# Kernel tuning notes

Hardware: AMD Instinct MI355X
Metric: run time of the kernel (lower is better)

Reference implementation:

```python
import jax, jax.numpy as jnp
import numpy as np

N_QUBITS = 4
N_LAYERS = 6
BATCH = 131072

# Pauli-Z expectation sign table: qubit q corresponds to bit (N_QUBITS-1-q) of the
# flattened state index (axis q+1 of the [B,2,2,2,2] state is most-significant first).
_idx = np.arange(2 ** N_QUBITS)
Z_SIGNS = jnp.asarray(1.0 - 2.0 * ((_idx[:, None] >> (N_QUBITS - 1 - np.arange(N_QUBITS))) & 1), dtype=jnp.float32)  # [16, 4]


def _apply_1q(state, U, q):
    # state: [B, 2,2,2,2]; U: [2,2] (shared) or [B,2,2] (per-sample)
    s = jnp.moveaxis(state, q + 1, -1)
    if U.ndim == 3:
        s = jnp.einsum('bij,b...j->b...i', U, s)
    else:
        s = jnp.einsum('ij,b...j->b...i', U, s)
    return jnp.moveaxis(s, -1, q + 1)


def _apply_cnot(state, c, t):
    # flip target axis on the control=1 slice
    s = jnp.moveaxis(state, (c + 1, t + 1), (-2, -1))
    s = jnp.concatenate([s[..., :1, :], s[..., 1:, ::-1]], axis=-2)
    return jnp.moveaxis(s, (-2, -1), (c + 1, t + 1))


def _rot(phi, theta, omega):
    # PennyLane Rot(phi, theta, omega) = RZ(omega) @ RY(theta) @ RZ(phi)
    ct = jnp.cos(theta / 2)
    st = jnp.sin(theta / 2)
    ep = jnp.exp(-0.5j * (phi + omega))  # e^{-i(phi+omega)/2}
    em = jnp.exp(0.5j * (phi - omega))   # e^{ i(phi-omega)/2}
    row0 = jnp.stack([ep * ct, -em * st])
    row1 = jnp.stack([jnp.conj(em) * st, jnp.conj(ep) * ct])
    return jnp.stack([row0, row1]).astype(jnp.complex64)


def _forward(inputs, rotations):
    B = inputs.shape[0]
    # |0...0> batched state
    state = jnp.zeros((B,) + (2,) * N_QUBITS, dtype=jnp.complex64)
    state = state.at[(slice(None),) + (0,) * N_QUBITS].set(1.0)

    # AngleEmbedding: RX(x_q) on wire q (per-sample gates)
    c = jnp.cos(inputs / 2)
    s = jnp.sin(inputs / 2)
    for q in range(N_QUBITS):
        U = jnp.stack([
            jnp.stack([c[:, q] + 0j, -1j * s[:, q]], axis=-1),
            jnp.stack([-1j * s[:, q], c[:, q] + 0j], axis=-1),
        ], axis=-2).astype(jnp.complex64)  # [B,2,2]
        state = _apply_1q(state, U, q)

    # StronglyEntanglingLayers
    for l in range(N_LAYERS):
        for q in range(N_QUBITS):
            state = _apply_1q(state, _rot(rotations[l, q, 0], rotations[l, q, 1], rotations[l, q, 2]), q)
        r = l % (N_QUBITS - 1) + 1  # default imprimitive range pattern
        for q in range(N_QUBITS):
            state = _apply_cnot(state, q, (q + r) % N_QUBITS)

    probs = (state.real ** 2 + state.imag ** 2).reshape(B, 2 ** N_QUBITS)  # [B,16]
    return (probs @ Z_SIGNS).astype(jnp.float32)  # [B, N_QUBITS] = <Z_q>


def setup_inputs() -> dict:
    key = jax.random.key(0)
    k1, k2 = jax.random.split(key)
    inputs = jax.random.normal(k1, (BATCH, N_QUBITS), dtype=jnp.float32)
    # keras 'random_uniform' initializer: U(-0.05, 0.05)
    rotations = jax.random.uniform(k2, (N_LAYERS, N_QUBITS, 3), dtype=jnp.float32, minval=-0.05, maxval=0.05)
    return {"inputs": inputs, "rotations": rotations}


def reference(inputs, rotations):
    return _forward(inputs, rotations)
```

## Files before the change

### kernel.cpp

```cpp
#include <hip/hip_runtime.h>
#include <math.h>

#define NQ 4
#define NL 6
#define DIM 16
#define BLOCK 256

__global__ __launch_bounds__(BLOCK) void vqc_kernel(
    const float* __restrict__ inputs,
    const float* __restrict__ rot,
    float* __restrict__ out,
    int batch)
{
    __shared__ float U[NL * NQ][8];

    const int tid = threadIdx.x;
    if (tid < NL * NQ) {
        float phi = rot[tid * 3 + 0];
        float theta = rot[tid * 3 + 1];
        float omega = rot[tid * 3 + 2];
        float st, ct;
        __sincosf(0.5f * theta, &st, &ct);
        float a = 0.5f * (phi + omega);
        float b = 0.5f * (phi - omega);
        float sa, ca, sb, cb;
        __sincosf(a, &sa, &ca);
        __sincosf(b, &sb, &cb);
        U[tid][0] = ca * ct;
        U[tid][1] = -sa * ct;
        U[tid][2] = -cb * st;
        U[tid][3] = -sb * st;
        U[tid][4] = cb * st;
        U[tid][5] = -sb * st;
        U[tid][6] = ca * ct;
        U[tid][7] = sa * ct;
    }
    __syncthreads();

    const int b = blockIdx.x * BLOCK + tid;
    if (b >= batch) return;

    const float4 x = ((const float4*)inputs)[b];
    float c[NQ], s[NQ];
    __sincosf(0.5f * x.x, &s[0], &c[0]);
    __sincosf(0.5f * x.y, &s[1], &c[1]);
    __sincosf(0.5f * x.z, &s[2], &c[2]);
    __sincosf(0.5f * x.w, &s[3], &c[3]);

    float sr[DIM], si[DIM];
#pragma unroll
    for (int i = 0; i < DIM; ++i) {
        float mag = (((i >> 3) & 1) ? s[0] : c[0])
                  * (((i >> 2) & 1) ? s[1] : c[1])
                  * (((i >> 1) & 1) ? s[2] : c[2])
                  * (((i >> 0) & 1) ? s[3] : c[3]);
        const int k = (((i >> 3) & 1) + ((i >> 2) & 1) + ((i >> 1) & 1) + (i & 1)) & 3;
        sr[i] = (k == 0) ? mag : ((k == 2) ? -mag : 0.0f);
        si[i] = (k == 1) ? -mag : ((k == 3) ? mag : 0.0f);
    }

#pragma unroll
    for (int l = 0; l < NL; ++l) {
#pragma unroll
        for (int q = 0; q < NQ; ++q) {
            const float* u = U[l * NQ + q];
            const float u00r = u[0], u00i = u[1], u01r = u[2], u01i = u[3];
            const float u10r = u[4], u10i = u[5], u11r = u[6], u11i = u[7];
            const int m = 1 << (3 - q);
#pragma unroll
            for (int i = 0; i < DIM; ++i) {
                if (!(i & m)) {
                    const int j = i | m;
                    const float a0r = sr[i], a0i = si[i];
                    const float a1r = sr[j], a1i = si[j];
                    sr[i] = u00r * a0r - u00i * a0i + u01r * a1r - u01i * a1i;
                    si[i] = u00r * a0i + u00i * a0r + u01r * a1i + u01i * a1r;
                    sr[j] = u10r * a0r - u10i * a0i + u11r * a1r - u11i * a1i;
                    si[j] = u10r * a0i + u10i * a0r + u11r * a1i + u11i * a1r;
                }
            }
        }
        const int r = l % (NQ - 1) + 1;
#pragma unroll
        for (int q = 0; q < NQ; ++q) {
            const int t = (q + r) & 3;
            const int cm = 1 << (3 - q);
            const int tm = 1 << (3 - t);
#pragma unroll
            for (int i = 0; i < DIM; ++i) {
                if ((i & cm) && !(i & tm)) {
                    const int j = i | tm;
                    float tr = sr[i]; sr[i] = sr[j]; sr[j] = tr;
                    float ti = si[i]; si[i] = si[j]; si[j] = ti;
                }
            }
        }
    }

    float e0 = 0.f, e1 = 0.f, e2 = 0.f, e3 = 0.f;
#pragma unroll
    for (int i = 0; i < DIM; ++i) {
        const float p = sr[i] * sr[i] + si[i] * si[i];
        e0 += ((i >> 3) & 1) ? -p : p;
        e1 += ((i >> 2) & 1) ? -p : p;
        e2 += ((i >> 1) & 1) ? -p : p;
        e3 += ((i >> 0) & 1) ? -p : p;
    }
    ((float4*)out)[b] = make_float4(e0, e1, e2, e3);
}

extern "C" void kernel_launch(void* const* d_in, const int* in_sizes, int n_in,
                              void* d_out, int out_size, void* d_ws, size_t ws_size,
                              hipStream_t stream) {
    const float* inputs = (const float*)d_in[0];
    const float* rot = (const float*)d_in[1];
    float* out = (float*)d_out;
    const int batch = in_sizes[0] / NQ;
    const int grid = (batch + BLOCK - 1) / BLOCK;
    vqc_kernel<<<grid, BLOCK, 0, stream>>>(inputs, rot, out, batch);
}
```

Measured before the change: 72.33 us.

## Precompute the full circuit unitary once and apply it per sample as a matvec

A small setup kernel simulates the fixed entangling circuit on each of the 16 basis states, producing a 16x16 complex unitary with the embedding phases folded in. It writes that unitary to workspace. The main kernel builds each sample's real product-state magnitudes and multiplies them by the unitary, 512 FMAs per sample, instead of applying 24 rotation gates and the CNOT permutations. The cost is an extra kernel launch and uniform global loads of the 512 matrix values in every thread.

Result: slower. 86.90 us (+20.1%).

```diff
diff --git a/kernel.cpp b/kernel.cpp
--- a/kernel.cpp
+++ b/kernel.cpp
@@ -6,66 +6,31 @@
 #define DIM 16
 #define BLOCK 256
 
-__global__ __launch_bounds__(BLOCK) void vqc_kernel(
-    const float* __restrict__ inputs,
-    const float* __restrict__ rot,
-    float* __restrict__ out,
-    int batch)
+__global__ void build_w_kernel(const float* __restrict__ rot,
+                               float* __restrict__ wr,
+                               float* __restrict__ wi)
 {
-    __shared__ float U[NL * NQ][8];
-
-    const int tid = threadIdx.x;
-    if (tid < NL * NQ) {
-        float phi = rot[tid * 3 + 0];
-        float theta = rot[tid * 3 + 1];
-        float omega = rot[tid * 3 + 2];
-        float st, ct;
-        __sincosf(0.5f * theta, &st, &ct);
-        float a = 0.5f * (phi + omega);
-        float b = 0.5f * (phi - omega);
-        float sa, ca, sb, cb;
-        __sincosf(a, &sa, &ca);
-        __sincosf(b, &sb, &cb);
-        U[tid][0] = ca * ct;
-        U[tid][1] = -sa * ct;
-        U[tid][2] = -cb * st;
-        U[tid][3] = -sb * st;
-        U[tid][4] = cb * st;
-        U[tid][5] = -sb * st;
-        U[tid][6] = ca * ct;
-        U[tid][7] = sa * ct;
-    }
-    __syncthreads();
-
-    const int b = blockIdx.x * BLOCK + tid;
-    if (b >= batch) return;
-
-    const float4 x = ((const float4*)inputs)[b];
-    float c[NQ], s[NQ];
-    __sincosf(0.5f * x.x, &s[0], &c[0]);
-    __sincosf(0.5f * x.y, &s[1], &c[1]);
-    __sincosf(0.5f * x.z, &s[2], &c[2]);
-    __sincosf(0.5f * x.w, &s[3], &c[3]);
+    const int c = threadIdx.x;
+    if (c >= DIM) return;
 
     float sr[DIM], si[DIM];
 #pragma unroll
-    for (int i = 0; i < DIM; ++i) {
-        float mag = (((i >> 3) & 1) ? s[0] : c[0])
-                  * (((i >> 2) & 1) ? s[1] : c[1])
-                  * (((i >> 1) & 1) ? s[2] : c[2])
-                  * (((i >> 0) & 1) ? s[3] : c[3]);
-        const int k = (((i >> 3) & 1) + ((i >> 2) & 1) + ((i >> 1) & 1) + (i & 1)) & 3;
-        sr[i] = (k == 0) ? mag : ((k == 2) ? -mag : 0.0f);
-        si[i] = (k == 1) ? -mag : ((k == 3) ? mag : 0.0f);
-    }
+    for (int i = 0; i < DIM; ++i) { sr[i] = (i == c) ? 1.0f : 0.0f; si[i] = 0.0f; }
 
 #pragma unroll
     for (int l = 0; l < NL; ++l) {
 #pragma unroll
         for (int q = 0; q < NQ; ++q) {
-            const float* u = U[l * NQ + q];
-            const float u00r = u[0], u00i = u[1], u01r = u[2], u01i = u[3];
-            const float u10r = u[4], u10i = u[5], u11r = u[6], u11i = u[7];
+            const float phi = rot[(l * NQ + q) * 3 + 0];
+            const float th  = rot[(l * NQ + q) * 3 + 1];
+            const float om  = rot[(l * NQ + q) * 3 + 2];
+            float st, ct; __sincosf(0.5f * th, &st, &ct);
+            float sa, ca; __sincosf(0.5f * (phi + om), &sa, &ca);
+            float sb, cb; __sincosf(0.5f * (phi - om), &sb, &cb);
+            const float u00r = ca * ct,  u00i = -sa * ct;
+            const float u01r = -cb * st, u01i = -sb * st;
+            const float u10r = cb * st,  u10i = -sb * st;
+            const float u11r = ca * ct,  u11i = sa * ct;
             const int m = 1 << (3 - q);
 #pragma unroll
             for (int i = 0; i < DIM; ++i) {
@@ -97,10 +62,56 @@
         }
     }
 
+    const int k = __popc(c) & 3;
+    const float pr = (k == 0) ? 1.0f : ((k == 2) ? -1.0f : 0.0f);
+    const float pm = (k == 3) ? 1.0f : ((k == 1) ? -1.0f : 0.0f);
+#pragma unroll
+    for (int i = 0; i < DIM; ++i) {
+        wr[c * DIM + i] = pr * sr[i] - pm * si[i];
+        wi[c * DIM + i] = pr * si[i] + pm * sr[i];
+    }
+}
+
+__global__ __launch_bounds__(BLOCK) void vqc_apply_kernel(
+    const float* __restrict__ inputs,
+    const float* __restrict__ wr,
+    const float* __restrict__ wi,
+    float* __restrict__ out,
+    int batch)
+{
+    const int b = blockIdx.x * BLOCK + threadIdx.x;
+    if (b >= batch) return;
+
+    const float4 x = ((const float4*)inputs)[b];
+    float c0, s0, c1, s1, c2, s2, c3, s3;
+    __sincosf(0.5f * x.x, &s0, &c0);
+    __sincosf(0.5f * x.y, &s1, &c1);
+    __sincosf(0.5f * x.z, &s2, &c2);
+    __sincosf(0.5f * x.w, &s3, &c3);
+
+    float m01[4] = {c0 * c1, c0 * s1, s0 * c1, s0 * s1};
+    float m23[4] = {c2 * c3, c2 * s3, s2 * c3, s2 * s3};
+    float mag[DIM];
+#pragma unroll
+    for (int i = 0; i < DIM; ++i) mag[i] = m01[i >> 2] * m23[i & 3];
+
+    float ar[DIM], ai[DIM];
+#pragma unroll
+    for (int i = 0; i < DIM; ++i) { ar[i] = 0.0f; ai[i] = 0.0f; }
+#pragma unroll
+    for (int c = 0; c < DIM; ++c) {
+        const float m = mag[c];
+#pragma unroll
+        for (int i = 0; i < DIM; ++i) {
+            ar[i] = fmaf(wr[c * DIM + i], m, ar[i]);
+            ai[i] = fmaf(wi[c * DIM + i], m, ai[i]);
+        }
+    }
+
     float e0 = 0.f, e1 = 0.f, e2 = 0.f, e3 = 0.f;
 #pragma unroll
     for (int i = 0; i < DIM; ++i) {
-        const float p = sr[i] * sr[i] + si[i] * si[i];
+        const float p = ar[i] * ar[i] + ai[i] * ai[i];
         e0 += ((i >> 3) & 1) ? -p : p;
         e1 += ((i >> 2) & 1) ? -p : p;
         e2 += ((i >> 1) & 1) ? -p : p;
@@ -115,7 +126,11 @@
     const float* inputs = (const float*)d_in[0];
     const float* rot = (const float*)d_in[1];
     float* out = (float*)d_out;
+    float* wr = (float*)d_ws;
+    float* wi = wr + DIM * DIM;
     const int batch = in_sizes[0] / NQ;
+
+    build_w_kernel<<<1, 64, 0, stream>>>(rot, wr, wi);
     const int grid = (batch + BLOCK - 1) / BLOCK;
-    vqc_kernel<<<grid, BLOCK, 0, stream>>>(inputs, rot, out, batch);
+    vqc_apply_kernel<<<grid, BLOCK, 0, stream>>>(inputs, wr, wi, out, batch);
 }
```
